# Performance work log

Hardware: AMD Instinct MI355X
Metric: run time of the kernel (lower is better)

## Reference

```python
import jax, jax.numpy as jnp
import numpy as np
from jax import lax

B, K, STATE_DIM, ENC_DIM, H = 4096, 32, 512, 128, 128
MLP_IN = 2 * ENC_DIM + 2 * H + STATE_DIM  # 1024
H1, H2 = 1024, 512
EPS = 1e-5

PARAM_NAMES = ['w_ih_f', 'w_hh_f', 'b_ih_f', 'b_hh_f',
               'w_ih_r', 'w_hh_r', 'b_ih_r', 'b_hh_r',
               'W1', 'b1', 'g1', 'be1', 'W2', 'b2', 'g2', 'be2', 'W3', 'b3']


def setup_inputs() -> dict:
    key = jax.random.key(0)
    ks = jax.random.split(key, 24)
    s = 0.05
    d = {
        'state':  jax.random.normal(ks[0], (B, STATE_DIM), jnp.float32),
        'action': jax.random.normal(ks[1], (B, K, ENC_DIM), jnp.float32),
        # BiLSTM (torch gate order i,f,g,o), forward and reverse directions
        'w_ih_f': jax.random.normal(ks[2], (4 * H, ENC_DIM), jnp.float32) * s,
        'w_hh_f': jax.random.normal(ks[3], (4 * H, H), jnp.float32) * s,
        'b_ih_f': jax.random.normal(ks[4], (4 * H,), jnp.float32) * s,
        'b_hh_f': jax.random.normal(ks[5], (4 * H,), jnp.float32) * s,
        'w_ih_r': jax.random.normal(ks[6], (4 * H, ENC_DIM), jnp.float32) * s,
        'w_hh_r': jax.random.normal(ks[7], (4 * H, H), jnp.float32) * s,
        'b_ih_r': jax.random.normal(ks[8], (4 * H,), jnp.float32) * s,
        'b_hh_r': jax.random.normal(ks[9], (4 * H,), jnp.float32) * s,
        # QNet MLP: Linear -> BN -> ReLU (x2, dropout treated as eval/identity) -> Linear
        'W1': jax.random.normal(ks[10], (H1, MLP_IN), jnp.float32) * s,
        'b1': jnp.zeros((H1,), jnp.float32),
        'g1': jnp.ones((H1,), jnp.float32),
        'be1': jnp.zeros((H1,), jnp.float32),
        'W2': jax.random.normal(ks[11], (H2, H1), jnp.float32) * s,
        'b2': jnp.zeros((H2,), jnp.float32),
        'g2': jnp.ones((H2,), jnp.float32),
        'be2': jnp.zeros((H2,), jnp.float32),
        'W3': jax.random.normal(ks[12], (1, H2), jnp.float32) * s,
        'b3': jnp.zeros((1,), jnp.float32),
    }
    return d


def _lstm_dir(V, w_ih, w_hh, b_ih, b_hh, reverse):
    # V: (B, K, D) -> hidden states (B, K, H)
    xs = jnp.swapaxes(V, 0, 1)  # (K, B, D)
    if reverse:
        xs = xs[::-1]
    x_proj = jnp.einsum('kbd,gd->kbg', xs, w_ih) + b_ih + b_hh  # (K, B, 4H)
    h0 = jnp.zeros((V.shape[0], w_hh.shape[1]), V.dtype)

    def step(carry, xp):
        h, c = carry
        gates = xp + h @ w_hh.T
        i, f, g, o = jnp.split(gates, 4, axis=-1)
        c = jax.nn.sigmoid(f) * c + jax.nn.sigmoid(i) * jnp.tanh(g)
        h = jax.nn.sigmoid(o) * jnp.tanh(c)
        return (h, c), h

    _, hs = lax.scan(step, (h0, h0), x_proj)
    if reverse:
        hs = hs[::-1]
    return jnp.swapaxes(hs, 0, 1)  # (B, K, H)


def _bn(x, gamma, beta):
    # training-mode BatchNorm1d over flattened batch dim, per feature
    mu = jnp.mean(x, axis=0)
    var = jnp.var(x, axis=0)
    return (x - mu) * lax.rsqrt(var + EPS) * gamma + beta


def _forward(state, action, w_ih_f, w_hh_f, b_ih_f, b_hh_f,
             w_ih_r, w_hh_r, b_ih_r, b_hh_r,
             W1, b1, g1, be1, W2, b2, g2, be2, W3, b3):
    V = action  # (B, K, D)
    Of = _lstm_dir(V, w_ih_f, w_hh_f, b_ih_f, b_hh_f, reverse=False)
    Or = _lstm_dir(V, w_ih_r, w_hh_r, b_ih_r, b_hh_r, reverse=True)
    O = jnp.concatenate([Of, Or], axis=-1)  # (B, K, 2H)

    # self-attention: scores = V V^T, softmax over keys, weighted sum of V
    attn = jax.nn.softmax(jnp.einsum('bkd,bld->bkl', V, V), axis=2)  # (B, K, K)
    A = jnp.einsum('bkl,bld->bkd', attn, V)  # (B, K, D)

    S = jnp.broadcast_to(state[:, None, :], (B, K, STATE_DIM))
    X = jnp.concatenate([S, O, V, A], axis=2).reshape(B * K, MLP_IN)

    h = jax.nn.relu(_bn(X @ W1.T + b1, g1, be1))
    h = jax.nn.relu(_bn(h @ W2.T + b2, g2, be2))
    Q = (h @ W3.T + b3).reshape(B, K)
    return Q


def reference(state, action, w_ih_f, w_hh_f, b_ih_f, b_hh_f,
              w_ih_r, w_hh_r, b_ih_r, b_hh_r,
              W1, b1, g1, be1, W2, b2, g2, be2, W3, b3):
    Q = _forward(state, action, w_ih_f, w_hh_f, b_ih_f, b_hh_f,
                 w_ih_r, w_hh_r, b_ih_r, b_hh_r,
                 W1, b1, g1, be1, W2, b2, g2, be2, W3, b3)
    params = [w_ih_f, w_hh_f, b_ih_f, b_hh_f, w_ih_r, w_hh_r, b_ih_r, b_hh_r,
              W1, b1, g1, be1, W2, b2, g2, be2, W3, b3]
    reg = sum(jnp.mean(p * p) for p in params)  # L2 regularization over module params
    return Q, reg
```

## Files before the change

kernel.cpp:

```cpp
#include <hip/hip_runtime.h>
#include <cstdint>

#define NROW 131072

typedef short bf16x8 __attribute__((ext_vector_type(8)));
typedef float f32x4 __attribute__((ext_vector_type(4)));

__device__ __forceinline__ unsigned short f2bf(float f){
  unsigned u = __builtin_bit_cast(unsigned, f);
  u += 0x7fffu + ((u >> 16) & 1u);
  return (unsigned short)(u >> 16);
}
__device__ __forceinline__ float bf2f(unsigned v){
  unsigned u = v << 16; return __builtin_bit_cast(float, u);
}
__device__ __forceinline__ float sigf(float x){ return 1.0f/(1.0f + __expf(-x)); }
__device__ __forceinline__ float tanh_fast(float x){ return 2.0f/(1.0f + __expf(-2.0f*x)) - 1.0f; }

#define WS_XOA  0x00000000UL
#define WS_Y2   0x06000000UL
#define WS_SM   0x0E000000UL
#define WS_YS   0x0E390000UL
#define NEED2   0x0F390000UL
#define SM_W1F  0x000000
#define SM_W2F  0x200000
#define SM_WIH  0x300000
#define SM_WHH  0x340000
#define SM_BIAS 0x380000
#define SM_STAT 0x381000
#define SM_A1   0x384000
#define SM_C1   0x385000
#define SM_A2   0x386000
#define SM_C2   0x386800

__device__ __forceinline__ void conv_frag(const float* __restrict__ src, unsigned short* __restrict__ dst,
                                          long g, long T){
  for (long i = g; i < 8192; i += T){
    int lane = (int)(i & 63);
    int blk  = (int)(i >> 6);
    int nt = blk >> 2, kt = blk & 3;
    const float* sp = src + (nt*16 + (lane&15))*128 + kt*32 + (lane>>4)*8;
    float4 a = *(const float4*)sp;
    float4 b = *(const float4*)(sp+4);
    uint4 o;
    o.x = (unsigned)f2bf(a.x) | ((unsigned)f2bf(a.y) << 16);
    o.y = (unsigned)f2bf(a.z) | ((unsigned)f2bf(a.w) << 16);
    o.z = (unsigned)f2bf(b.x) | ((unsigned)f2bf(b.y) << 16);
    o.w = (unsigned)f2bf(b.z) | ((unsigned)f2bf(b.w) << 16);
    *((uint4*)dst + i) = o;
  }
}

__global__ __launch_bounds__(256) void prep_kernel(
    const float* __restrict__ wihf, const float* __restrict__ whhf,
    const float* __restrict__ bihf, const float* __restrict__ bhhf,
    const float* __restrict__ wihr, const float* __restrict__ whhr,
    const float* __restrict__ bihr, const float* __restrict__ bhhr,
    const float* __restrict__ W1, const float* __restrict__ W2,
    unsigned short* __restrict__ W1f, unsigned short* __restrict__ W2f,
    unsigned short* __restrict__ wih, unsigned short* __restrict__ whh,
    float* __restrict__ bias){
  const long T = (long)gridDim.x * 256;
  const long g = (long)blockIdx.x * 256 + threadIdx.x;
  for (long s = g; s < 131072; s += T){
    int lane = (int)(s & 63);
    long t = s >> 6;
    int c16 = (int)(t & 7);
    long t2 = t >> 3;
    int ksub = (int)(t2 & 1);
    long t3 = t2 >> 1;
    int kb = (int)(t3 & 15);
    int chunk = (int)(t3 >> 4);
    const float* sp = W1 + (long)(chunk*128 + c16*16 + (lane&15))*1024 + kb*64 + ksub*32 + (lane>>4)*8;
    float4 a = *(const float4*)sp;
    float4 b = *(const float4*)(sp+4);
    uint4 o;
    o.x = (unsigned)f2bf(a.x) | ((unsigned)f2bf(a.y) << 16);
    o.y = (unsigned)f2bf(a.z) | ((unsigned)f2bf(a.w) << 16);
    o.z = (unsigned)f2bf(b.x) | ((unsigned)f2bf(b.y) << 16);
    o.w = (unsigned)f2bf(b.z) | ((unsigned)f2bf(b.w) << 16);
    *((uint4*)W1f + s) = o;
  }
  for (long s = g; s < 65536; s += T){
    int lane = (int)(s & 63);
    long t = s >> 6;
    int c16 = (int)(t & 31);
    long t2 = t >> 5;
    int ksub = (int)(t2 & 1);
    long t3 = t2 >> 1;
    int kh = (int)(t3 & 1);
    int nt = (int)(t3 >> 1);
    const float* sp = W2 + (long)(c16*16 + (lane&15))*1024 + nt*128 + kh*64 + ksub*32 + (lane>>4)*8;
    float4 a = *(const float4*)sp;
    float4 b = *(const float4*)(sp+4);
    uint4 o;
    o.x = (unsigned)f2bf(a.x) | ((unsigned)f2bf(a.y) << 16);
    o.y = (unsigned)f2bf(a.z) | ((unsigned)f2bf(a.w) << 16);
    o.z = (unsigned)f2bf(b.x) | ((unsigned)f2bf(b.y) << 16);
    o.w = (unsigned)f2bf(b.z) | ((unsigned)f2bf(b.w) << 16);
    *((uint4*)W2f + s) = o;
  }
  conv_frag(wihf, wih, g, T);
  conv_frag(whhf, whh, g, T);
  conv_frag(wihr, wih + 65536, g, T);
  conv_frag(whhr, whh + 65536, g, T);
  for (long i = g; i < 512; i += T){
    bias[i]       = bihf[i] + bhhf[i];
    bias[512 + i] = bihr[i] + bhhr[i];
  }
}

__global__ __launch_bounds__(256) void reg_kernel(
    const float* p0, const float* p1, const float* p2, const float* p3,
    const float* p4, const float* p5, const float* p6, const float* p7,
    const float* p8, const float* p9, const float* p10, const float* p11,
    const float* p12, const float* p13, const float* p14, const float* p15,
    const float* p16, const float* p17, float* __restrict__ out){
  const int tid = threadIdx.x;
  const long T = (long)gridDim.x * 256;
  const long g = (long)blockIdx.x * 256 + tid;
  float local = 0.f;
#define RLOOP(P, SZ) for (long i = g; i < (SZ); i += T){ float v = (P)[i]; local += v*v*(1.0f/(float)(SZ)); }
  RLOOP(p0, 65536) RLOOP(p1, 65536) RLOOP(p2, 512) RLOOP(p3, 512)
  RLOOP(p4, 65536) RLOOP(p5, 65536) RLOOP(p6, 512) RLOOP(p7, 512)
  RLOOP(p8, 1048576) RLOOP(p9, 1024) RLOOP(p10, 1024) RLOOP(p11, 1024)
  RLOOP(p12, 524288) RLOOP(p13, 512) RLOOP(p14, 512) RLOOP(p15, 512)
  RLOOP(p16, 512) RLOOP(p17, 1)
#undef RLOOP
  #pragma unroll
  for (int off=32; off>=1; off>>=1) local += __shfl_down(local, off);
  __shared__ float wsum[4];
  if ((tid & 63) == 0) wsum[tid>>6] = local;
  __syncthreads();
  if (tid == 0) atomicAdd(out, wsum[0]+wsum[1]+wsum[2]+wsum[3]);
}

__global__ __launch_bounds__(256, 1) void lstm_kernel(
    const float* __restrict__ action,
    const unsigned short* __restrict__ wih_all,
    const unsigned short* __restrict__ whh_all,
    const float* __restrict__ bias_all,
    unsigned short* __restrict__ XOA){
  const int dir = blockIdx.y;
  const int b0 = blockIdx.x * 32;
  const unsigned short* __restrict__ wih = wih_all + dir * 65536;
  const unsigned short* __restrict__ whh = whh_all + dir * 65536;
  const float* __restrict__ bias = bias_all + dir * 512;
  __shared__ __align__(16) unsigned short whl[65536];
  __shared__ __align__(16) unsigned short lh[32*136];
  const int tid = threadIdx.x;
  const int lane = tid & 63;
  const int wv = tid >> 6;
  const int l15 = lane & 15, l4 = lane >> 4;
  for (int i = tid; i < 8192; i += 256)
    *((uint4*)whl + i) = *((const uint4*)whh + i);
  for (int i = tid; i < 32*136; i += 256) lh[i] = 0;
  bf16x8 wr[4][2][4];
  #pragma unroll
  for (int G2=0;G2<4;G2++)
    #pragma unroll
    for (int qq=0;qq<2;qq++){
      const int nt = G2*8 + 2*wv + qq;
      #pragma unroll
      for (int kt=0;kt<4;kt++)
        wr[G2][qq][kt] = *(const bf16x8*)&wih[((nt*4 + kt)*64 + lane)*8];
    }
  float bias_r[2][4];
  #pragma unroll
  for (int qq=0;qq<2;qq++)
    #pragma unroll
    for (int G2=0;G2<4;G2++)
      bias_r[qq][G2] = bias[G2*128 + (2*wv+qq)*16 + l15];
  f32x4 cst[2][2];
  #pragma unroll
  for (int mt=0;mt<2;mt++)
    #pragma unroll
    for (int qq=0;qq<2;qq++){ f32x4 z = {0.f,0.f,0.f,0.f}; cst[mt][qq] = z; }
  __syncthreads();

  for (int s = 0; s < 32; s++){
    const int korig = dir ? (31 - s) : s;
    bf16x8 ha[2][4];
    #pragma unroll
    for (int mt=0;mt<2;mt++)
      #pragma unroll
      for (int kt=0;kt<4;kt++)
        ha[mt][kt] = *(const bf16x8*)&lh[(mt*16 + l15)*136 + kt*32 + l4*8];
    __syncthreads();
    bf16x8 xa[2][4];
    #pragma unroll
    for (int mt=0;mt<2;mt++)
      #pragma unroll
      for (int kt=0;kt<4;kt++){
        const float* sp = action + ((long)(b0 + mt*16 + l15)*32 + korig)*128 + kt*32 + l4*8;
        float4 a = *(const float4*)sp;
        float4 b = *(const float4*)(sp + 4);
        bf16x8 t;
        t[0]=(short)f2bf(a.x); t[1]=(short)f2bf(a.y); t[2]=(short)f2bf(a.z); t[3]=(short)f2bf(a.w);
        t[4]=(short)f2bf(b.x); t[5]=(short)f2bf(b.y); t[6]=(short)f2bf(b.z); t[7]=(short)f2bf(b.w);
        xa[mt][kt] = t;
      }
    f32x4 acc[2][2][4];
    #pragma unroll
    for (int mt=0;mt<2;mt++)
      #pragma unroll
      for (int qq=0;qq<2;qq++)
        #pragma unroll
        for (int G2=0;G2<4;G2++){
          float bb = bias_r[qq][G2];
          f32x4 z = {bb,bb,bb,bb};
          acc[mt][qq][G2] = z;
        }
    #pragma unroll
    for (int G2=0;G2<4;G2++)
      #pragma unroll
      for (int qq=0;qq<2;qq++){
        const int nt = G2*8 + 2*wv + qq;
        #pragma unroll
        for (int kt=0;kt<4;kt++){
          acc[0][qq][G2] = __builtin_amdgcn_mfma_f32_16x16x32_bf16(xa[0][kt], wr[G2][qq][kt], acc[0][qq][G2], 0,0,0);
          acc[1][qq][G2] = __builtin_amdgcn_mfma_f32_16x16x32_bf16(xa[1][kt], wr[G2][qq][kt], acc[1][qq][G2], 0,0,0);
        }
        #pragma unroll
        for (int kt=0;kt<4;kt++){
          bf16x8 bw = *(const bf16x8*)&whl[((nt*4 + kt)*64 + lane)*8];
          acc[0][qq][G2] = __builtin_amdgcn_mfma_f32_16x16x32_bf16(ha[0][kt], bw, acc[0][qq][G2], 0,0,0);
          acc[1][qq][G2] = __builtin_amdgcn_mfma_f32_16x16x32_bf16(ha[1][kt], bw, acc[1][qq][G2], 0,0,0);
        }
      }
    #pragma unroll
    for (int mt=0;mt<2;mt++)
      #pragma unroll
      for (int qq=0;qq<2;qq++){
        const int hcol = (2*wv+qq)*16 + l15;
        #pragma unroll
        for (int r=0;r<4;r++){
          float iv = acc[mt][qq][0][r];
          float fv = acc[mt][qq][1][r];
          float gv = acc[mt][qq][2][r];
          float ov = acc[mt][qq][3][r];
          float c = cst[mt][qq][r];
          c = sigf(fv)*c + sigf(iv)*tanh_fast(gv);
          float h = sigf(ov)*tanh_fast(c);
          cst[mt][qq][r] = c;
          const int row = mt*16 + l4*4 + r;
          unsigned short hb = f2bf(h);
          lh[row*136 + hcol] = hb;
          XOA[((long)(b0+row)*32 + korig)*384 + dir*128 + hcol] = hb;
        }
      }
    __syncthreads();
  }
}

__global__ __launch_bounds__(256) void attn_pack(
    const float* __restrict__ action,
    unsigned short* __restrict__ XOA){
  const int b = blockIdx.x;
  const int tid = threadIdx.x;
  __shared__ __align__(16) float V[32][132];
  __shared__ __align__(16) float attw[32][33];
  const float* __restrict__ src = action + (long)b*32*128;
  for (int i = tid; i < 1024; i += 256){
    int r = i >> 5, c4 = i & 31;
    *(float4*)&V[r][c4*4] = *(const float4*)&src[r*128 + c4*4];
  }
  __syncthreads();
  const int i = tid >> 3, j0 = tid & 7;
  float sacc[4] = {0.f,0.f,0.f,0.f};
  for (int c=0;c<32;c++){
    float4 vi = *(const float4*)&V[i][c*4];
    #pragma unroll
    for (int jj=0;jj<4;jj++){
      float4 vj = *(const float4*)&V[j0 + jj*8][c*4];
      sacc[jj] += vi.x*vj.x + vi.y*vj.y + vi.z*vj.z + vi.w*vj.w;
    }
  }
  float m = fmaxf(fmaxf(sacc[0],sacc[1]), fmaxf(sacc[2],sacc[3]));
  #pragma unroll
  for (int off=1; off<8; off<<=1) m = fmaxf(m, __shfl_xor(m, off));
  float e0 = __expf(sacc[0]-m), e1 = __expf(sacc[1]-m), e2 = __expf(sacc[2]-m), e3 = __expf(sacc[3]-m);
  float ssum = e0+e1+e2+e3;
  #pragma unroll
  for (int off=1; off<8; off<<=1) ssum += __shfl_xor(ssum, off);
  float inv = 1.0f / ssum;
  attw[i][j0] = e0*inv; attw[i][j0+8] = e1*inv; attw[i][j0+16] = e2*inv; attw[i][j0+24] = e3*inv;
  __syncthreads();
  const int d0 = (tid & 7) * 16;
  float a[16];
  #pragma unroll
  for (int t=0;t<16;t++) a[t]=0.f;
  for (int j=0;j<32;j++){
    float w = attw[i][j];
    #pragma unroll
    for (int dd=0;dd<4;dd++){
      float4 v = *(const float4*)&V[j][d0 + dd*4];
      a[dd*4+0] += w*v.x; a[dd*4+1] += w*v.y; a[dd*4+2] += w*v.z; a[dd*4+3] += w*v.w;
    }
  }
  unsigned short* rowp = XOA + ((long)b*32 + i)*384;
  #pragma unroll
  for (int t=0;t<8;t++){
    ushort2 u; u.x = f2bf(a[t*2]); u.y = f2bf(a[t*2+1]);
    *(ushort2*)(rowp + 256 + d0 + t*2) = u;
  }
}

__global__ __launch_bounds__(256, 3) void ys_kernel(
    const float* __restrict__ state,
    const unsigned short* __restrict__ W1f,
    float* __restrict__ Ys){
  __shared__ __align__(16) unsigned short lA[2][8192];
  const int tid = threadIdx.x;
  const int lane = tid & 63;
  const long m0 = (long)blockIdx.x * 128;
  const int chunk = blockIdx.y;
  const int mh = (tid >> 6) >> 1, nh = (tid >> 6) & 1;
  f32x4 acc[4][4];
  #pragma unroll
  for (int a=0;a<4;a++)
    #pragma unroll
    for (int b=0;b<4;b++){ f32x4 z = {0.f,0.f,0.f,0.f}; acc[a][b] = z; }

  bf16x8 sa[4];
  const int srow = tid >> 3;
  const int sg   = (tid & 7) * 8;

  auto load_g = [&](int kb){
    const int k0 = kb << 6;
    #pragma unroll
    for (int i=0;i<4;i++){
      long r = m0 + i*32 + srow;
      const float* sp = state + r*512 + k0 + sg;
      float4 a = *(const float4*)sp;
      float4 b = *(const float4*)(sp + 4);
      bf16x8 t;
      t[0]=(short)f2bf(a.x); t[1]=(short)f2bf(a.y); t[2]=(short)f2bf(a.z); t[3]=(short)f2bf(a.w);
      t[4]=(short)f2bf(b.x); t[5]=(short)f2bf(b.y); t[6]=(short)f2bf(b.z); t[7]=(short)f2bf(b.w);
      sa[i] = t;
    }
  };
  auto write_l = [&](int buf){
    #pragma unroll
    for (int i=0;i<4;i++){
      int r = i*32 + srow;
      int j = ((tid&7) ^ (r & 7)) * 8;
      *(bf16x8*)&lA[buf][r*64 + j] = sa[i];
    }
  };
  auto compute = [&](int buf, int kb){
    #pragma unroll
    for (int ksub=0; ksub<2; ksub++){
      const unsigned short* wb = W1f + (((chunk*16 + kb)*2 + ksub)*8 + nh*4)*512 + lane*8;
      bf16x8 af[4], bg[4];
      #pragma unroll
      for (int nt=0;nt<4;nt++) bg[nt] = *(const bf16x8*)(wb + nt*512);
      #pragma unroll
      for (int mt=0;mt<4;mt++){
        int r = mh*64 + mt*16 + (lane&15);
        int p = (ksub*4 + (lane>>4)) ^ (r&7);
        af[mt] = *(const bf16x8*)&lA[buf][r*64 + p*8];
      }
      #pragma unroll
      for (int mt=0;mt<4;mt++)
        #pragma unroll
        for (int nt=0;nt<4;nt++)
          acc[mt][nt] = __builtin_amdgcn_mfma_f32_16x16x32_bf16(af[mt], bg[nt], acc[mt][nt], 0,0,0);
    }
  };

  load_g(0);
  write_l(0);
  __syncthreads();
  for (int kb = 0; kb < 8; kb++){
    if (kb + 1 < 8) load_g(kb+1);
    compute(kb & 1, kb);
    if (kb + 1 < 8) write_l((kb+1) & 1);
    __syncthreads();
  }

  #pragma unroll
  for (int nt=0; nt<4; nt++){
    int col = chunk*128 + nh*64 + nt*16 + (lane & 15);
    #pragma unroll
    for (int mt=0; mt<4; mt++){
      #pragma unroll
      for (int r=0;r<4;r++){
        long row = m0 + mh*64 + mt*16 + (lane>>4)*4 + r;
        Ys[row*1024 + col] = acc[mt][nt][r];
      }
    }
  }
}

__global__ __launch_bounds__(256, 2) void gemm1_stats(
    const float* __restrict__ action,
    const unsigned short* __restrict__ XOA,
    const unsigned short* __restrict__ W1f,
    const float* __restrict__ Ys,
    float* __restrict__ bnsum, float* __restrict__ bnsq){
  __shared__ __align__(16) unsigned short stage[4][8192];
  const int tid = threadIdx.x;
  const int lane = tid & 63;
  const int w = tid >> 6;
  const long m0 = (long)blockIdx.x * 64;
  const int rowg = w >> 1, colg = w & 1;

  #pragma unroll
  for (int kbp = 4; kbp < 8; kbp++){
    #pragma unroll
    for (int i=0;i<4;i++){
      int ch = i*256 + tid;
      int row = ch >> 4, kc = ch & 15;
      long R = m0 + row;
      bf16x8 t;
      if (kbp == 6){
        const float* sp = action + R*128 + kc*8;
        float4 a = *(const float4*)sp;
        float4 b = *(const float4*)(sp + 4);
        t[0]=(short)f2bf(a.x); t[1]=(short)f2bf(a.y); t[2]=(short)f2bf(a.z); t[3]=(short)f2bf(a.w);
        t[4]=(short)f2bf(b.x); t[5]=(short)f2bf(b.y); t[6]=(short)f2bf(b.z); t[7]=(short)f2bf(b.w);
      } else {
        int col = (kbp < 6) ? ((kbp-4)*128) : 256;
        t = *(const bf16x8*)&XOA[R*384 + col + kc*8];
      }
      int j = (kc ^ (row & 7)) * 8;
      *(bf16x8*)&stage[kbp-4][row*128 + j] = t;
    }
  }
  __syncthreads();

  const long rbb = m0 >> 5;
  for (int chunk = 0; chunk < 8; chunk++){
    f32x4 acc[2][4];
    #pragma unroll
    for (int rt=0;rt<2;rt++){
      long rb = rbb + ((rowg*32 + rt*16) >> 5);
      #pragma unroll
      for (int ct=0;ct<4;ct++){
        int col = chunk*128 + colg*64 + ct*16 + (lane & 15);
        float v = Ys[rb*1024 + col];
        f32x4 z = {v,v,v,v}; acc[rt][ct] = z;
      }
    }
    #pragma unroll
    for (int kbp=4; kbp<8; kbp++){
      #pragma unroll
      for (int ks4=0; ks4<4; ks4++){
        const int kb = kbp*2 + (ks4 >> 1);
        const int ksub = ks4 & 1;
        const unsigned short* wb = W1f + (((chunk*16 + kb)*2 + ksub)*8 + colg*4)*512 + lane*8;
        bf16x8 af[2], bg[4];
        #pragma unroll
        for (int ct=0;ct<4;ct++) bg[ct] = *(const bf16x8*)(wb + ct*512);
        #pragma unroll
        for (int rt=0;rt<2;rt++){
          int r = rowg*32 + rt*16 + (lane&15);
          int p = (ks4*4 + (lane>>4)) ^ (r&7);
          af[rt] = *(const bf16x8*)&stage[kbp-4][r*128 + p*8];
        }
        __builtin_amdgcn_s_setprio(1);
        #pragma unroll
        for (int rt=0;rt<2;rt++)
          #pragma unroll
          for (int ct=0;ct<4;ct++)
            acc[rt][ct] = __builtin_amdgcn_mfma_f32_16x16x32_bf16(af[rt], bg[ct], acc[rt][ct], 0,0,0);
        __builtin_amdgcn_s_setprio(0);
      }
    }
    #pragma unroll
    for (int ct=0;ct<4;ct++){
      int col = chunk*128 + colg*64 + ct*16 + (lane & 15);
      float s = 0.f, q = 0.f;
      #pragma unroll
      for (int rt=0;rt<2;rt++)
        #pragma unroll
        for (int r=0;r<4;r++){
          float v = acc[rt][ct][r];
          s += v; q += v*v;
        }
      s += __shfl_down(s, 32); q += __shfl_down(q, 32);
      s += __shfl_down(s, 16); q += __shfl_down(q, 16);
      if (lane < 16){
        atomicAdd(&bnsum[col], s);
        atomicAdd(&bnsq[col], q);
      }
    }
  }
}

__global__ void bn_finalize(const float* __restrict__ sum, const float* __restrict__ sq,
                            const float* __restrict__ gamma, const float* __restrict__ beta,
                            float* __restrict__ a, float* __restrict__ c, int N){
  int i = blockIdx.x*256 + threadIdx.x;
  if (i >= N) return;
  const float invM = 1.0f / 131072.0f;
  float mu = sum[i]*invM;
  float var = sq[i]*invM - mu*mu;
  float s = rsqrtf(var + 1e-5f) * gamma[i];
  a[i] = s;
  c[i] = beta[i] - mu*s;
}

__global__ __launch_bounds__(256, 2) void gemm12(
    const float* __restrict__ action,
    const unsigned short* __restrict__ XOA,
    const unsigned short* __restrict__ W1f,
    const unsigned short* __restrict__ W2f,
    const float* __restrict__ Ys,
    const float* __restrict__ a1, const float* __restrict__ c1,
    unsigned short* __restrict__ Y2,
    float* __restrict__ bnsum, float* __restrict__ bnsq){
  __shared__ __align__(16) unsigned short stage[4][8192];
  __shared__ __align__(16) unsigned short h1c[8192];
  const int tid = threadIdx.x;
  const int lane = tid & 63;
  const int w = tid >> 6;
  const long m0 = (long)blockIdx.x * 64;
  const int rowgA = w >> 1, colgA = w & 1;
  const int rgB = w >> 1, cgB = w & 1;

  #pragma unroll
  for (int kbp = 4; kbp < 8; kbp++){
    #pragma unroll
    for (int i=0;i<4;i++){
      int ch = i*256 + tid;
      int row = ch >> 4, kc = ch & 15;
      long R = m0 + row;
      bf16x8 t;
      if (kbp == 6){
        const float* sp = action + R*128 + kc*8;
        float4 a = *(const float4*)sp;
        float4 b = *(const float4*)(sp + 4);
        t[0]=(short)f2bf(a.x); t[1]=(short)f2bf(a.y); t[2]=(short)f2bf(a.z); t[3]=(short)f2bf(a.w);
        t[4]=(short)f2bf(b.x); t[5]=(short)f2bf(b.y); t[6]=(short)f2bf(b.z); t[7]=(short)f2bf(b.w);
      } else {
        int col = (kbp < 6) ? ((kbp-4)*128) : 256;
        t = *(const bf16x8*)&XOA[R*384 + col + kc*8];
      }
      int j = (kc ^ (row & 7)) * 8;
      *(bf16x8*)&stage[kbp-4][row*128 + j] = t;
    }
  }

  f32x4 acc2[2][16];
  #pragma unroll
  for (int a=0;a<2;a++)
    #pragma unroll
    for (int b=0;b<16;b++){ f32x4 z = {0.f,0.f,0.f,0.f}; acc2[a][b] = z; }

  const long rbb = m0 >> 5;
  __syncthreads();

  for (int nt = 0; nt < 8; nt++){
    f32x4 acc1[2][4];
    #pragma unroll
    for (int rt=0;rt<2;rt++){
      long rb = rbb + ((rowgA*32 + rt*16) >> 5);
      #pragma unroll
      for (int ct=0;ct<4;ct++){
        int col = nt*128 + colgA*64 + ct*16 + (lane & 15);
        float v = Ys[rb*1024 + col];
        f32x4 z = {v,v,v,v}; acc1[rt][ct] = z;
      }
    }
    #pragma unroll
    for (int kbp=4; kbp<8; kbp++){
      #pragma unroll
      for (int ks4=0; ks4<4; ks4++){
        const int kb = kbp*2 + (ks4 >> 1);
        const int ksub = ks4 & 1;
        const unsigned short* wb = W1f + (((nt*16 + kb)*2 + ksub)*8 + colgA*4)*512 + lane*8;
        bf16x8 af[2], bg[4];
        #pragma unroll
        for (int ct=0;ct<4;ct++) bg[ct] = *(const bf16x8*)(wb + ct*512);
        #pragma unroll
        for (int rt=0;rt<2;rt++){
          int r = rowgA*32 + rt*16 + (lane&15);
          int p = (ks4*4 + (lane>>4)) ^ (r&7);
          af[rt] = *(const bf16x8*)&stage[kbp-4][r*128 + p*8];
        }
        __builtin_amdgcn_s_setprio(1);
        #pragma unroll
        for (int rt=0;rt<2;rt++)
          #pragma unroll
          for (int ct=0;ct<4;ct++)
            acc1[rt][ct] = __builtin_amdgcn_mfma_f32_16x16x32_bf16(af[rt], bg[ct], acc1[rt][ct], 0,0,0);
        __builtin_amdgcn_s_setprio(0);
      }
    }

    __syncthreads();

    #pragma unroll
    for (int ct=0;ct<4;ct++){
      int lcol = colgA*64 + ct*16 + (lane&15);
      float av = a1[nt*128 + lcol];
      float cv = c1[nt*128 + lcol];
      #pragma unroll
      for (int rt=0;rt<2;rt++)
        #pragma unroll
        for (int r=0;r<4;r++){
          int row = rowgA*32 + rt*16 + (lane>>4)*4 + r;
          float h = fmaxf(fmaf(acc1[rt][ct][r], av, cv), 0.f);
          int sc = (lcol & 7) | ((((lcol >> 3) ^ (row & 7)) & 15) << 3);
          h1c[row*128 + sc] = f2bf(h);
        }
    }
    __syncthreads();

    #pragma unroll
    for (int kh=0;kh<2;kh++){
      #pragma unroll
      for (int ksub=0;ksub<2;ksub++){
        bf16x8 af[2];
        #pragma unroll
        for (int rt=0;rt<2;rt++){
          int row = rgB*32 + rt*16 + (lane&15);
          int g0 = kh*8 + ksub*4 + (lane>>4);
          int gs = g0 ^ (row & 7);
          af[rt] = *(const bf16x8*)&h1c[row*128 + gs*8];
        }
        #pragma unroll
        for (int cth=0;cth<2;cth++){
          const unsigned short* wb = W2f + ((((nt*2 + kh)*2 + ksub)*32) + cgB*16 + cth*8)*512 + lane*8;
          bf16x8 bg[8];
          #pragma unroll
          for (int ct=0;ct<8;ct++) bg[ct] = *(const bf16x8*)(wb + ct*512);
          __builtin_amdgcn_s_setprio(1);
          #pragma unroll
          for (int rt=0;rt<2;rt++)
            #pragma unroll
            for (int ct=0;ct<8;ct++)
              acc2[rt][cth*8+ct] = __builtin_amdgcn_mfma_f32_16x16x32_bf16(af[rt], bg[ct], acc2[rt][cth*8+ct], 0,0,0);
          __builtin_amdgcn_s_setprio(0);
        }
      }
    }
  }

  #pragma unroll
  for (int ct=0;ct<16;ct++){
    int col = cgB*256 + ct*16 + (lane&15);
    float s = 0.f, q = 0.f;
    #pragma unroll
    for (int rt=0;rt<2;rt++)
      #pragma unroll
      for (int r=0;r<4;r++){
        long row = m0 + rgB*32 + rt*16 + (lane>>4)*4 + r;
        unsigned short ub = f2bf(acc2[rt][ct][r]);
        Y2[row*512 + col] = ub;
        float vq = bf2f(ub);
        s += vq; q += vq*vq;
      }
    s += __shfl_down(s, 32); q += __shfl_down(q, 32);
    s += __shfl_down(s, 16); q += __shfl_down(q, 16);
    if (lane < 16){
      atomicAdd(&bnsum[col], s);
      atomicAdd(&bnsq[col], q);
    }
  }
}

__global__ __launch_bounds__(256) void final_kernel(
    const unsigned short* __restrict__ Y2,
    const float* __restrict__ a2, const float* __restrict__ c2,
    const float* __restrict__ W3, const float* __restrict__ b3, float* __restrict__ Q){
  const int tid = threadIdx.x;
  const int lane = tid & 63, wv = tid >> 6;
  const int wid = blockIdx.x*4 + wv;
  const int cb = lane*8;
  float4 a0 = *(const float4*)&a2[cb], a1 = *(const float4*)&a2[cb+4];
  float4 c0 = *(const float4*)&c2[cb], c1 = *(const float4*)&c2[cb+4];
  float4 w0 = *(const float4*)&W3[cb], w1 = *(const float4*)&W3[cb+4];
  const float b3v = b3[0];
  for (long row = wid; row < NROW; row += 4096){
    uint4 u = *(const uint4*)(Y2 + row*512 + cb);
    float y0 = bf2f(u.x & 0xffffu), y1 = bf2f(u.x >> 16);
    float y2 = bf2f(u.y & 0xffffu), y3 = bf2f(u.y >> 16);
    float y4 = bf2f(u.z & 0xffffu), y5 = bf2f(u.z >> 16);
    float y6 = bf2f(u.w & 0xffffu), y7 = bf2f(u.w >> 16);
    float t = fmaxf(fmaf(y0,a0.x,c0.x),0.f)*w0.x
            + fmaxf(fmaf(y1,a0.y,c0.y),0.f)*w0.y
            + fmaxf(fmaf(y2,a0.z,c0.z),0.f)*w0.z
            + fmaxf(fmaf(y3,a0.w,c0.w),0.f)*w0.w
            + fmaxf(fmaf(y4,a1.x,c1.x),0.f)*w1.x
            + fmaxf(fmaf(y5,a1.y,c1.y),0.f)*w1.y
            + fmaxf(fmaf(y6,a1.z,c1.z),0.f)*w1.z
            + fmaxf(fmaf(y7,a1.w,c1.w),0.f)*w1.w;
    #pragma unroll
    for (int off=32; off>=1; off>>=1) t += __shfl_down(t, off);
    if (lane == 0) Q[row] = t + b3v;
  }
}

extern "C" void kernel_launch(void* const* d_in, const int* in_sizes, int n_in,
                              void* d_out, int out_size, void* d_ws, size_t ws_size,
                              hipStream_t stream){
  (void)in_sizes; (void)n_in; (void)out_size;
  if (ws_size < NEED2) return;

  const float* state  = (const float*)d_in[0];
  const float* action = (const float*)d_in[1];
  const float* w_ih_f = (const float*)d_in[2];
  const float* w_hh_f = (const float*)d_in[3];
  const float* b_ih_f = (const float*)d_in[4];
  const float* b_hh_f = (const float*)d_in[5];
  const float* w_ih_r = (const float*)d_in[6];
  const float* w_hh_r = (const float*)d_in[7];
  const float* b_ih_r = (const float*)d_in[8];
  const float* b_hh_r = (const float*)d_in[9];
  const float* W1  = (const float*)d_in[10];
  const float* b1  = (const float*)d_in[11];
  const float* g1  = (const float*)d_in[12];
  const float* be1 = (const float*)d_in[13];
  const float* W2  = (const float*)d_in[14];
  const float* b2  = (const float*)d_in[15];
  const float* g2  = (const float*)d_in[16];
  const float* be2 = (const float*)d_in[17];
  const float* W3  = (const float*)d_in[18];
  const float* b3  = (const float*)d_in[19];
  (void)b1; (void)b2;

  char* ws = (char*)d_ws;
  unsigned short* XOA = (unsigned short*)(ws + WS_XOA);
  unsigned short* Y2  = (unsigned short*)(ws + WS_Y2);
  float* Ysp = (float*)(ws + WS_YS);
  char* sm = ws + WS_SM;
  unsigned short* W1f = (unsigned short*)(sm + SM_W1F);
  unsigned short* W2f = (unsigned short*)(sm + SM_W2F);
  unsigned short* wih = (unsigned short*)(sm + SM_WIH);
  unsigned short* whh = (unsigned short*)(sm + SM_WHH);
  float* bias   = (float*)(sm + SM_BIAS);
  float* bnsum1 = (float*)(sm + SM_STAT);
  float* bnsq1  = (float*)(sm + SM_STAT + 0x1000);
  float* bnsum2 = (float*)(sm + SM_STAT + 0x2000);
  float* bnsq2  = (float*)(sm + SM_STAT + 0x2800);
  float* a1 = (float*)(sm + SM_A1);
  float* c1 = (float*)(sm + SM_C1);
  float* a2 = (float*)(sm + SM_A2);
  float* c2 = (float*)(sm + SM_C2);
  float* qout = (float*)d_out;
  float* regout = qout + 131072;

  hipMemsetAsync(bnsum1, 0, 0x3000, stream);
  hipMemsetAsync(regout, 0, 4, stream);

  prep_kernel<<<1024, 256, 0, stream>>>(w_ih_f, w_hh_f, b_ih_f, b_hh_f,
                                        w_ih_r, w_hh_r, b_ih_r, b_hh_r,
                                        W1, W2, W1f, W2f, wih, whh, bias);
  reg_kernel<<<256, 256, 0, stream>>>(w_ih_f, w_hh_f, b_ih_f, b_hh_f,
                                      w_ih_r, w_hh_r, b_ih_r, b_hh_r,
                                      W1, b1, g1, be1, W2, b2, g2, be2, W3, b3, regout);
  ys_kernel<<<dim3(32, 8), 256, 0, stream>>>(state, W1f, Ysp);
  lstm_kernel<<<dim3(128,2), 256, 0, stream>>>(action, wih, whh, bias, XOA);
  attn_pack<<<4096, 256, 0, stream>>>(action, XOA);
  gemm1_stats<<<2048, 256, 0, stream>>>(action, XOA, W1f, Ysp, bnsum1, bnsq1);
  bn_finalize<<<4, 256, 0, stream>>>(bnsum1, bnsq1, g1, be1, a1, c1, 1024);
  gemm12<<<2048, 256, 0, stream>>>(action, XOA, W1f, W2f, Ysp, a1, c1, Y2, bnsum2, bnsq2);
  bn_finalize<<<2, 256, 0, stream>>>(bnsum2, bnsq2, g2, be2, a2, c2, 512);
  final_kernel<<<1024, 256, 0, stream>>>(Y2, a2, c2, W3, b3, qout);
}
```

Before: 1.226 ms.

## Split LSTM gate tiles across eight waves instead of four per block

The LSTM kernel now runs 512 threads per block. Each of the eight waves owns one 16-column hidden tile instead of two, so per-wave MFMA work, weight registers and accumulators are halved. This is meant to shorten the serial per-timestep critical path of the recurrence by adding more waves to hide latency. The cost is more waves contending for the shared-memory W_hh reads and the per-step barriers. The launch_bounds hint of two blocks per CU is likely unreachable, because the kernel uses about 137KB of shared memory.

```diff
diff --git a/kernel.cpp b/kernel.cpp
--- a/kernel.cpp
+++ b/kernel.cpp
@@ -135,7 +135,7 @@
   if (tid == 0) atomicAdd(out, wsum[0]+wsum[1]+wsum[2]+wsum[3]);
 }
 
-__global__ __launch_bounds__(256, 1) void lstm_kernel(
+__global__ __launch_bounds__(512, 2) void lstm_kernel(
     const float* __restrict__ action,
     const unsigned short* __restrict__ wih_all,
     const unsigned short* __restrict__ whh_all,
@@ -152,30 +152,22 @@
   const int lane = tid & 63;
   const int wv = tid >> 6;
   const int l15 = lane & 15, l4 = lane >> 4;
-  for (int i = tid; i < 8192; i += 256)
+  for (int i = tid; i < 8192; i += 512)
     *((uint4*)whl + i) = *((const uint4*)whh + i);
-  for (int i = tid; i < 32*136; i += 256) lh[i] = 0;
-  bf16x8 wr[4][2][4];
+  for (int i = tid; i < 32*136; i += 512) lh[i] = 0;
+  bf16x8 wr[4][4];
   #pragma unroll
   for (int G2=0;G2<4;G2++)
     #pragma unroll
-    for (int qq=0;qq<2;qq++){
-      const int nt = G2*8 + 2*wv + qq;
-      #pragma unroll
-      for (int kt=0;kt<4;kt++)
-        wr[G2][qq][kt] = *(const bf16x8*)&wih[((nt*4 + kt)*64 + lane)*8];
-    }
-  float bias_r[2][4];
-  #pragma unroll
-  for (int qq=0;qq<2;qq++)
-    #pragma unroll
-    for (int G2=0;G2<4;G2++)
-      bias_r[qq][G2] = bias[G2*128 + (2*wv+qq)*16 + l15];
-  f32x4 cst[2][2];
-  #pragma unroll
-  for (int mt=0;mt<2;mt++)
-    #pragma unroll
-    for (int qq=0;qq<2;qq++){ f32x4 z = {0.f,0.f,0.f,0.f}; cst[mt][qq] = z; }
+    for (int kt=0;kt<4;kt++)
+      wr[G2][kt] = *(const bf16x8*)&wih[(((G2*8 + wv)*4 + kt)*64 + lane)*8];
+  float bias_r[4];
+  #pragma unroll
+  for (int G2=0;G2<4;G2++)
+    bias_r[G2] = bias[G2*128 + wv*16 + l15];
+  f32x4 cst[2];
+  #pragma unroll
+  for (int mt=0;mt<2;mt++){ f32x4 z = {0.f,0.f,0.f,0.f}; cst[mt] = z; }
   __syncthreads();
 
   for (int s = 0; s < 32; s++){
@@ -200,55 +192,49 @@
         t[4]=(short)f2bf(b.x); t[5]=(short)f2bf(b.y); t[6]=(short)f2bf(b.z); t[7]=(short)f2bf(b.w);
         xa[mt][kt] = t;
       }
-    f32x4 acc[2][2][4];
+    f32x4 acc[2][4];
     #pragma unroll
     for (int mt=0;mt<2;mt++)
       #pragma unroll
-      for (int qq=0;qq<2;qq++)
-        #pragma unroll
-        for (int G2=0;G2<4;G2++){
-          float bb = bias_r[qq][G2];
-          f32x4 z = {bb,bb,bb,bb};
-          acc[mt][qq][G2] = z;
-        }
-    #pragma unroll
-    for (int G2=0;G2<4;G2++)
-      #pragma unroll
-      for (int qq=0;qq<2;qq++){
-        const int nt = G2*8 + 2*wv + qq;
-        #pragma unroll
-        for (int kt=0;kt<4;kt++){
-          acc[0][qq][G2] = __builtin_amdgcn_mfma_f32_16x16x32_bf16(xa[0][kt], wr[G2][qq][kt], acc[0][qq][G2], 0,0,0);
-          acc[1][qq][G2] = __builtin_amdgcn_mfma_f32_16x16x32_bf16(xa[1][kt], wr[G2][qq][kt], acc[1][qq][G2], 0,0,0);
-        }
-        #pragma unroll
-        for (int kt=0;kt<4;kt++){
-          bf16x8 bw = *(const bf16x8*)&whl[((nt*4 + kt)*64 + lane)*8];
-          acc[0][qq][G2] = __builtin_amdgcn_mfma_f32_16x16x32_bf16(ha[0][kt], bw, acc[0][qq][G2], 0,0,0);
-          acc[1][qq][G2] = __builtin_amdgcn_mfma_f32_16x16x32_bf16(ha[1][kt], bw, acc[1][qq][G2], 0,0,0);
-        }
-      }
-    #pragma unroll
-    for (int mt=0;mt<2;mt++)
-      #pragma unroll
-      for (int qq=0;qq<2;qq++){
-        const int hcol = (2*wv+qq)*16 + l15;
-        #pragma unroll
-        for (int r=0;r<4;r++){
-          float iv = acc[mt][qq][0][r];
-          float fv = acc[mt][qq][1][r];
-          float gv = acc[mt][qq][2][r];
-          float ov = acc[mt][qq][3][r];
-          float c = cst[mt][qq][r];
-          c = sigf(fv)*c + sigf(iv)*tanh_fast(gv);
-          float h = sigf(ov)*tanh_fast(c);
-          cst[mt][qq][r] = c;
-          const int row = mt*16 + l4*4 + r;
-          unsigned short hb = f2bf(h);
-          lh[row*136 + hcol] = hb;
-          XOA[((long)(b0+row)*32 + korig)*384 + dir*128 + hcol] = hb;
-        }
-      }
+      for (int G2=0;G2<4;G2++){
+        float bb = bias_r[G2];
+        f32x4 z = {bb,bb,bb,bb};
+        acc[mt][G2] = z;
+      }
+    #pragma unroll
+    for (int G2=0;G2<4;G2++){
+      const int nt = G2*8 + wv;
+      #pragma unroll
+      for (int kt=0;kt<4;kt++){
+        acc[0][G2] = __builtin_amdgcn_mfma_f32_16x16x32_bf16(xa[0][kt], wr[G2][kt], acc[0][G2], 0,0,0);
+        acc[1][G2] = __builtin_amdgcn_mfma_f32_16x16x32_bf16(xa[1][kt], wr[G2][kt], acc[1][G2], 0,0,0);
+      }
+      #pragma unroll
+      for (int kt=0;kt<4;kt++){
+        bf16x8 bw = *(const bf16x8*)&whl[((nt*4 + kt)*64 + lane)*8];
+        acc[0][G2] = __builtin_amdgcn_mfma_f32_16x16x32_bf16(ha[0][kt], bw, acc[0][G2], 0,0,0);
+        acc[1][G2] = __builtin_amdgcn_mfma_f32_16x16x32_bf16(ha[1][kt], bw, acc[1][G2], 0,0,0);
+      }
+    }
+    const int hcol = wv*16 + l15;
+    #pragma unroll
+    for (int mt=0;mt<2;mt++){
+      #pragma unroll
+      for (int r=0;r<4;r++){
+        float iv = acc[mt][0][r];
+        float fv = acc[mt][1][r];
+        float gv = acc[mt][2][r];
+        float ov = acc[mt][3][r];
+        float c = cst[mt][r];
+        c = sigf(fv)*c + sigf(iv)*tanh_fast(gv);
+        float h = sigf(ov)*tanh_fast(c);
+        cst[mt][r] = c;
+        const int row = mt*16 + l4*4 + r;
+        unsigned short hb = f2bf(h);
+        lh[row*136 + hcol] = hb;
+        XOA[((long)(b0+row)*32 + korig)*384 + dir*128 + hcol] = hb;
+      }
+    }
     __syncthreads();
   }
 }
@@ -753,7 +739,7 @@
                                       w_ih_r, w_hh_r, b_ih_r, b_hh_r,
                                       W1, b1, g1, be1, W2, b2, g2, be2, W3, b3, regout);
   ys_kernel<<<dim3(32, 8), 256, 0, stream>>>(state, W1f, Ysp);
-  lstm_kernel<<<dim3(128,2), 256, 0, stream>>>(action, wih, whh, bias, XOA);
+  lstm_kernel<<<dim3(128,2), 512, 0, stream>>>(action, wih, whh, bias, XOA);
   attn_pack<<<4096, 256, 0, stream>>>(action, XOA);
   gemm1_stats<<<2048, 256, 0, stream>>>(action, XOA, W1f, Ysp, bnsum1, bnsq1);
   bn_finalize<<<4, 256, 0, stream>>>(bnsum1, bnsq1, g1, be1, a1, c1, 1024);
```

After: 1.232 ms. Within noise of the previous version (+0.5%).
